# Optimization experiments

Measured on AMD Instinct MI355X. Metric: run time of the kernel, lower is better.

Reference implementation:

```python
import jax, jax.numpy as jnp
import numpy as np

B, S, IN, META, H, G = 256, 1024, 4, 4, 256, 768  # G = 3*H, gate order (r, z, n)


def setup_inputs() -> dict:
    key = jax.random.key(0)
    ks = jax.random.split(key, 12)
    sc = 1.0 / np.sqrt(H)
    return {
        "x": jax.random.normal(ks[0], (B, S, IN), jnp.float32),
        "meta": jax.random.normal(ks[1], (B, META), jnp.float32),
        "W_ih0": jax.random.normal(ks[2], (G, IN + META), jnp.float32) * sc,
        "W_hh0": jax.random.normal(ks[3], (G, H), jnp.float32) * sc,
        "b_ih0": jax.random.normal(ks[4], (G,), jnp.float32) * sc,
        "b_hh0": jax.random.normal(ks[5], (G,), jnp.float32) * sc,
        "W_ih1": jax.random.normal(ks[6], (G, H), jnp.float32) * sc,
        "W_hh1": jax.random.normal(ks[7], (G, H), jnp.float32) * sc,
        "b_ih1": jax.random.normal(ks[8], (G,), jnp.float32) * sc,
        "b_hh1": jax.random.normal(ks[9], (G,), jnp.float32) * sc,
        "fc_W": jax.random.normal(ks[10], (1, H), jnp.float32) * sc,
        "fc_b": jax.random.normal(ks[11], (1,), jnp.float32) * sc,
    }


def _gru_layer(x_seq, W_ih, W_hh, b_ih, b_hh):
    # x_seq: [B, S, F] -> outputs [B, S, H]. PyTorch GRU, gate order (r, z, n).
    h_dim = W_hh.shape[1]
    # Precompute input projections for all timesteps (one big GEMM).
    xg = jnp.einsum('bsf,gf->sbg', x_seq, W_ih) + b_ih  # [S, B, 3H]

    def step(h, xg_t):
        hg = h @ W_hh.T + b_hh  # [B, 3H]
        r = jax.nn.sigmoid(xg_t[:, :h_dim] + hg[:, :h_dim])
        z = jax.nn.sigmoid(xg_t[:, h_dim:2 * h_dim] + hg[:, h_dim:2 * h_dim])
        n = jnp.tanh(xg_t[:, 2 * h_dim:] + r * hg[:, 2 * h_dim:])
        h_new = (1.0 - z) * n + z * h
        return h_new, h_new

    h0 = jnp.zeros((x_seq.shape[0], h_dim), x_seq.dtype)
    _, out = jax.lax.scan(step, h0, xg)  # out: [S, B, H]
    return jnp.transpose(out, (1, 0, 2))


def reference(x, meta, W_ih0, W_hh0, b_ih0, b_hh0, W_ih1, W_hh1, b_ih1, b_hh1, fc_W, fc_b):
    # Tile meta across time and concat to features: [B, S, IN+META]
    meta_t = jnp.broadcast_to(meta[:, None, :], (x.shape[0], x.shape[1], meta.shape[-1]))
    xin = jnp.concatenate([x, meta_t], axis=-1)
    h1 = _gru_layer(xin, W_ih0, W_hh0, b_ih0, b_hh0)
    h2 = _gru_layer(h1, W_ih1, W_hh1, b_ih1, b_hh1)
    last = h2[:, -1, :]  # [B, H]
    return last @ fc_W.T + fc_b  # [B, 1]
```

## Files before the change

### kernel.cpp

```cpp
#include <hip/hip_runtime.h>
#include <hip/hip_fp16.h>


#define SCH 32
#define NCH 32

typedef _Float16 half8 __attribute__((ext_vector_type(8)));
typedef _Float16 half4_t __attribute__((ext_vector_type(4)));
typedef float f32x4 __attribute__((ext_vector_type(4)));

__device__ __forceinline__ float rcp_(float x) {
#if __has_builtin(__builtin_amdgcn_rcpf)
    return __builtin_amdgcn_rcpf(x);
#else
    return 1.f / x;
#endif
}
__device__ __forceinline__ float exp2_(float x) {
#if __has_builtin(__builtin_amdgcn_exp2f)
    return __builtin_amdgcn_exp2f(x);
#else
    return exp2f(x);
#endif
}
__device__ __forceinline__ float sigf(float v) {
    return rcp_(1.f + exp2_(v * -1.442695041f));
}
__device__ __forceinline__ float tanh_(float v) {
    return 1.f - 2.f * rcp_(1.f + exp2_(v * 2.885390082f));
}

__device__ __forceinline__ void lds_barrier() {
    __asm__ volatile("s_waitcnt lgkmcnt(0)" ::: "memory");
    __builtin_amdgcn_s_barrier();
}

__global__ __launch_bounds__(256) void prep_kernel(
    const float* __restrict__ Whh0, const float* __restrict__ Whh1,
    const float* __restrict__ Wih1,
    _Float16* __restrict__ Wfrag0, _Float16* __restrict__ Wfrag1,
    _Float16* __restrict__ Wi1frag) {
    int tid = blockIdx.x * 256 + threadIdx.x;
    int mat = tid / 24576;
    int r   = tid % 24576;
    int kt   = r / 3072;
    int rem  = r % 3072;
    int nt   = rem >> 6;
    int lane = rem & 63;
    int n = nt * 16 + (lane & 15);
    int k = kt * 32 + (lane >> 4) * 8;
    const float* src = (mat == 0 ? Whh0 : (mat == 1 ? Whh1 : Wih1)) + n * 256 + k;
    _Float16* dst = (mat == 0 ? Wfrag0 : (mat == 1 ? Wfrag1 : Wi1frag)) + (size_t)r * 8;
#pragma unroll
    for (int j = 0; j < 8; j++) dst[j] = (_Float16)src[j];
}

__global__
__attribute__((amdgpu_flat_work_group_size(512, 512), amdgpu_waves_per_eu(2, 2)))
void mega_kernel(
    const float* __restrict__ x, const float* __restrict__ meta,
    const float* __restrict__ Wih0, const float* __restrict__ bih0,
    const float* __restrict__ bhh0,
    const _Float16* __restrict__ Wfrag0, const _Float16* __restrict__ Wfrag1,
    const _Float16* __restrict__ Wi1frag,
    const float* __restrict__ bih1, const float* __restrict__ bhh1,
    float* __restrict__ hst0, float* __restrict__ hst1,
    _Float16* __restrict__ hout0, _Float16* __restrict__ hout1,
    _Float16* __restrict__ xg0a, _Float16* __restrict__ xg0b,
    _Float16* __restrict__ xg1a, _Float16* __restrict__ xg1b,
    const float* __restrict__ fcW, const float* __restrict__ fcb,
    float* __restrict__ out, int k) {
    __shared__ __align__(16) char smem[27648];
    const int bid = blockIdx.x;
    const int tid = threadIdx.x;

    if (bid < 64) {
        const int role = bid >> 5;
        const int cc = role ? k - 2 : k;
        if (cc < 0 || cc >= NCH) return;
        const _Float16* Wfrag = role ? Wfrag1 : Wfrag0;
        const float* bhh      = role ? bhh1 : bhh0;
        const _Float16* xgt   = role ? ((cc & 1) ? xg1b : xg1a)
                                     : ((cc & 1) ? xg0b : xg0a);
        float* hstate         = role ? hst1 : hst0;
        _Float16* hof         = (cc & 1) ? hout1 : hout0;
        const bool doHout = (role == 0);
        const bool doFC   = (role == 1) && (cc == NCH - 1);

        _Float16* shA = (_Float16*)smem;
        float* shred  = (float*)smem;
        const int w = tid >> 6, lane = tid & 63;
        const int lm = lane & 15;
        const int hi = lane >> 5;
        const int blk = bid & 31;

        int nt[6];
        nt[0] = 2 * w;      nt[1] = 2 * w + 1;
        nt[2] = 16 + 2 * w; nt[3] = 17 + 2 * w;
        nt[4] = 32 + 2 * w; nt[5] = 33 + 2 * w;

        half8 Bf[48];
#pragma unroll
        for (int kt = 0; kt < 8; kt++)
#pragma unroll
            for (int t = 0; t < 6; t++)
                Bf[kt * 6 + t] = *(const half8*)(Wfrag + (size_t)((kt * 48 + nt[t]) * 64 + lane) * 8);

        const float bbnA = bhh[512 + 32 * w + lm];
        const float bbnB = bhh[512 + 32 * w + 16 + lm];

        float hreg[4];
        if (cc == 0) {
#pragma unroll
            for (int r = 0; r < 4; r++) hreg[r] = 0.f;
        } else {
            f32x4 v0 = *(const f32x4*)(hstate + ((size_t)(blk * 8 + w) * 64 + lane) * 4);
#pragma unroll
            for (int r = 0; r < 4; r++) hreg[r] = v0[r];
        }

        const int rdo = (lane >> 4) * 64 + (lane & 7) * 8;
        const int wb2 = w * 256 + (hi * 2 + (lm >> 3)) * 64 + ((lane >> 4) & 1) * 32 + (lm & 7);

#pragma unroll
        for (int r = 0; r < 4; r++) shA[wb2 + r * 8] = (_Float16)hreg[r];

        const _Float16* xp = xgt + (size_t)(blk * 8 + w) * 768 + lane * 4;
        _Float16* hop = hof + (size_t)(blk * 8 + w) * 256 + lane * 8;

        half4_t xcb[2][3];
        xcb[0][0] = *(const half4_t*)(xp);
        xcb[0][1] = *(const half4_t*)(xp + 256);
        xcb[0][2] = *(const half4_t*)(xp + 512);
        xp += 196608;

        __syncthreads();

#define GRU_STEP(SIDE)                                                            \
    {                                                                             \
        xcb[(SIDE) ^ 1][0] = *(const half4_t*)(xp);                               \
        xcb[(SIDE) ^ 1][1] = *(const half4_t*)(xp + 256);                         \
        xcb[(SIDE) ^ 1][2] = *(const half4_t*)(xp + 512);                         \
        xp += 196608;                                                             \
        f32x4 acc[6];                                                             \
        acc[0] = acc[1] = acc[2] = acc[3] = (f32x4){0.f, 0.f, 0.f, 0.f};          \
        acc[4] = (f32x4){bbnA, bbnA, bbnA, bbnA};                                 \
        acc[5] = (f32x4){bbnB, bbnB, bbnB, bbnB};                                 \
        _Pragma("unroll")                                                         \
        for (int kt = 0; kt < 8; kt++) {                                          \
            half8 af = *(const half8*)(shA + (SIDE) * 2048 + kt * 256 + rdo);     \
            _Pragma("unroll")                                                     \
            for (int t = 0; t < 6; t++)                                           \
                acc[t] = __builtin_amdgcn_mfma_f32_16x16x32_f16(                  \
                    af, Bf[kt * 6 + t], acc[t], 0, 0, 0);                         \
        }                                                                         \
        f32x4 aR = hi ? acc[1] : acc[0];                                          \
        f32x4 aZ = hi ? acc[3] : acc[2];                                          \
        f32x4 aN = hi ? acc[5] : acc[4];                                          \
        half4_t xR = xcb[SIDE][0];                                                \
        half4_t xZ = xcb[SIDE][1];                                                \
        half4_t xN = xcb[SIDE][2];                                                \
        _Pragma("unroll")                                                         \
        for (int r = 0; r < 4; r++) {                                             \
            float rr = sigf((float)xR[r] + aR[r]);                                \
            float zz = sigf((float)xZ[r] + aZ[r]);                                \
            float nn = tanh_((float)xN[r] + rr * aN[r]);                          \
            hreg[r] = nn + zz * (hreg[r] - nn);                                   \
        }                                                                         \
        _Pragma("unroll")                                                         \
        for (int r = 0; r < 4; r++)                                               \
            shA[((SIDE) ^ 1) * 2048 + wb2 + r * 8] = (_Float16)hreg[r];           \
        if (doHout && lane < 32) {                                                \
            half8 v = *(const half8*)(shA + ((SIDE) ^ 1) * 2048 +                 \
                                      w * 256 + lane * 8);                        \
            *(half8*)hop = v;                                                     \
        }                                                                         \
        hop += 65536;                                                             \
        lds_barrier();                                                            \
    }

        for (int s2 = 0; s2 < SCH; s2 += 2) {
            GRU_STEP(0);
            GRU_STEP(1);
        }
#undef GRU_STEP

        {
            f32x4 v0;
#pragma unroll
            for (int r = 0; r < 4; r++) v0[r] = hreg[r];
            *(f32x4*)(hstate + ((size_t)(blk * 8 + w) * 64 + lane) * 4) = v0;
        }

        if (doFC) {
            float fw = fcW[32 * w + hi * 16 + lm];
            f32x4 pv;
#pragma unroll
            for (int r = 0; r < 4; r++) pv[r] = hreg[r] * fw;
            __syncthreads();
            *(f32x4*)(shred + (size_t)(w * 64 + lane) * 4) = pv;
            __syncthreads();
            if (tid < 8) {
                int qq = tid >> 2, rr2 = tid & 3;
                float a = fcb[0];
                for (int ww = 0; ww < 8; ww++)
                    for (int l2 = 0; l2 < 16; l2++)
                        a += shred[(ww * 64 + qq * 16 + l2) * 4 + rr2]
                           + shred[(ww * 64 + 32 + qq * 16 + l2) * 4 + rr2];
                out[blk * 8 + tid] = a;
            }
        }
    } else if (bid < 96) {
        const int cb = k + 1;
        if (cb < 0 || cb >= NCH) return;
        _Float16* xg0 = (cb & 1) ? xg0b : xg0a;
        const int fb = bid - 64;
        float* Wb = (float*)smem;
        for (int i = tid; i < 6912; i += 512)
            Wb[i] = (i < 6144) ? Wih0[i]
                               : (bih0[i - 6144] + ((i - 6144) < 512 ? bhh0[i - 6144] : 0.f));
        __syncthreads();
        const int sub = tid >> 8;
        const int t = tid & 255;
        const int w = t >> 5, l32 = t & 31;
        const int qc = l32 >> 4, lm = l32 & 15;

        float Wr[6][8], br[6];
#pragma unroll
        for (int g3 = 0; g3 < 3; g3++)
#pragma unroll
            for (int tp = 0; tp < 2; tp++) {
                int n = g3 * 256 + 32 * w + 16 * tp + lm;
                int j6 = g3 * 2 + tp;
#pragma unroll
                for (int kk = 0; kk < 8; kk++) Wr[j6][kk] = Wb[n * 8 + kk];
                br[j6] = Wb[6144 + n];
            }
        const int b0 = fb * 8 + qc * 4;
        float4 mv[4];
#pragma unroll
        for (int r = 0; r < 4; r++) mv[r] = *(const float4*)(meta + (b0 + r) * 4);

        for (int sl = 0; sl < 16; sl++) {
            int s_local = sub * 16 + sl;
            int s = cb * SCH + s_local;
            float4 xv[4];
#pragma unroll
            for (int r = 0; r < 4; r++)
                xv[r] = *(const float4*)(x + ((size_t)(b0 + r) * 1024 + s) * 4);
            half4_t o[2][3];
#pragma unroll
            for (int g3 = 0; g3 < 3; g3++)
#pragma unroll
                for (int tp = 0; tp < 2; tp++) {
                    int j6 = g3 * 2 + tp;
#pragma unroll
                    for (int r = 0; r < 4; r++) {
                        float v = br[j6]
                            + xv[r].x * Wr[j6][0] + xv[r].y * Wr[j6][1]
                            + xv[r].z * Wr[j6][2] + xv[r].w * Wr[j6][3]
                            + mv[r].x * Wr[j6][4] + mv[r].y * Wr[j6][5]
                            + mv[r].z * Wr[j6][6] + mv[r].w * Wr[j6][7];
                        o[tp][g3][r] = (_Float16)v;
                    }
                }
            _Float16* dst = xg0 + ((size_t)(s_local * 32 + fb) * 8 + w) * 768;
#pragma unroll
            for (int tp = 0; tp < 2; tp++) {
                int slot4 = (l32 + tp * 32) * 4;
#pragma unroll
                for (int g3 = 0; g3 < 3; g3++)
                    *(half4_t*)(dst + g3 * 256 + slot4) = o[tp][g3];
            }
        }
    } else {
        const int c1 = k - 1;
        if (c1 < 0 || c1 >= NCH) return;
        const _Float16* hof = (c1 & 1) ? hout1 : hout0;
        _Float16* xg1 = (c1 & 1) ? xg1b : xg1a;
        const int fb = bid - 96;
        const int sub = tid >> 8;
        const int t = tid & 255;
        const int wv = t >> 6, lane = t & 63;
        const int q = lane >> 4, lm = lane & 15;
        const int asel = (lane >> 3) & 1;
        const int cidx = (lane >> 4) * 8 + (lane & 7);

        float bias[12];
#pragma unroll
        for (int j = 0; j < 12; j++) {
            int n = (wv * 12 + j) * 16 + lm;
            bias[j] = bih1[n] + (n < 512 ? bhh1[n] : 0.f);
        }
        const int t16 = (fb * 2 + sub) * 2;
        f32x4 acc[2][12] = {};
#pragma unroll
        for (int kt = 0; kt < 8; kt++) {
            half8 af[2], bf[12];
#pragma unroll
            for (int i = 0; i < 2; i++) {
                int tt = t16 + i, s = tt >> 4, bt = tt & 15;
                af[i] = *(const half8*)(hof +
                    (((size_t)(s * 32 + bt * 2 + asel) * 8 + kt) * 32 + cidx) * 8);
            }
#pragma unroll
            for (int j = 0; j < 12; j++)
                bf[j] = *(const half8*)(Wi1frag + (size_t)((kt * 48 + wv * 12 + j) * 64 + lane) * 8);
#pragma unroll
            for (int i = 0; i < 2; i++)
#pragma unroll
                for (int j = 0; j < 12; j++)
                    acc[i][j] = __builtin_amdgcn_mfma_f32_16x16x32_f16(af[i], bf[j], acc[i][j], 0, 0, 0);
        }
#pragma unroll
        for (int i = 0; i < 2; i++) {
            int tt = t16 + i, s = tt >> 4, bt = tt & 15;
            int blk = bt * 2 + (q >> 1), qc2 = q & 1;
#pragma unroll
            for (int j = 0; j < 12; j++) {
                int n = (wv * 12 + j) * 16 + lm;
                int g3 = n >> 8, nn = n & 255;
                int wc = nn >> 5, tp = (nn >> 4) & 1, lmc = nn & 15;
                half4_t v;
#pragma unroll
                for (int r = 0; r < 4; r++) v[r] = (_Float16)(acc[i][j][r] + bias[j]);
                *(half4_t*)(xg1 + ((size_t)(s * 32 + blk) * 8 + wc) * 768
                                 + g3 * 256 + (qc2 * 16 + lmc + tp * 32) * 4) = v;
            }
        }
    }
}

extern "C" void kernel_launch(void* const* d_in, const int* in_sizes, int n_in,
                              void* d_out, int out_size, void* d_ws, size_t ws_size,
                              hipStream_t stream) {
    const float* x    = (const float*)d_in[0];
    const float* meta = (const float*)d_in[1];
    const float* Wih0 = (const float*)d_in[2];
    const float* Whh0 = (const float*)d_in[3];
    const float* bih0 = (const float*)d_in[4];
    const float* bhh0 = (const float*)d_in[5];
    const float* Wih1 = (const float*)d_in[6];
    const float* Whh1 = (const float*)d_in[7];
    const float* bih1 = (const float*)d_in[8];
    const float* bhh1 = (const float*)d_in[9];
    const float* fcW  = (const float*)d_in[10];
    const float* fcb  = (const float*)d_in[11];
    float* out = (float*)d_out;

    char* ws = (char*)d_ws;
    _Float16* Wfrag0  = (_Float16*)(ws + 0);
    _Float16* Wfrag1  = (_Float16*)(ws + 393216);
    _Float16* Wi1frag = (_Float16*)(ws + 786432);
    float*    hst0    = (float*)(ws + 1179648);
    float*    hst1    = (float*)(ws + 1441792);
    _Float16* hout0   = (_Float16*)(ws + 1703936);
    _Float16* xg0a    = (_Float16*)(ws + 5898240);
    _Float16* xg0b    = (_Float16*)(ws + 18481152);
    _Float16* xg1a    = (_Float16*)(ws + 31064064);
    _Float16* xg1b    = (_Float16*)(ws + 43646976);
    _Float16* hout1   = (_Float16*)(ws + 56229888);

    prep_kernel<<<288, 256, 0, stream>>>(Whh0, Whh1, Wih1, Wfrag0, Wfrag1, Wi1frag);

    for (int k = -1; k <= NCH + 1; k++) {
        mega_kernel<<<224, 512, 0, stream>>>(
            x, meta, Wih0, bih0, bhh0, Wfrag0, Wfrag1, Wi1frag, bih1, bhh1,
            hst0, hst1, hout0, hout1, xg0a, xg0b, xg1a, xg1b, fcW, fcb, out, k);
    }
}
```

Before: 1.660 ms.

## Split MFMA accumulator chains and write hidden state directly from registers

The recurrent step now splits the K-loop into two independent accumulator sets, so the dependent MFMA chain is half as long, and sums them afterward. Layer-0 hidden outputs are written by every lane straight from registers in the accumulator layout, instead of being read back from LDS by half the lanes. The layer-1 input-projection blocks stage their hidden tile into padded shared memory to turn the A-operand loads into LDS reads. This trades a few extra vector adds and a larger LDS footprint for a shorter critical path per step and simpler global access.

After: 2.870 ms. 72.9% more time.

```diff
diff --git a/kernel.cpp b/kernel.cpp
--- a/kernel.cpp
+++ b/kernel.cpp
@@ -70,7 +70,7 @@
     _Float16* __restrict__ xg1a, _Float16* __restrict__ xg1b,
     const float* __restrict__ fcW, const float* __restrict__ fcb,
     float* __restrict__ out, int k) {
-    __shared__ __align__(16) char smem[27648];
+    __shared__ __align__(16) char smem[33792];
     const int bid = blockIdx.x;
     const int tid = threadIdx.x;
 
@@ -126,7 +126,7 @@
         for (int r = 0; r < 4; r++) shA[wb2 + r * 8] = (_Float16)hreg[r];
 
         const _Float16* xp = xgt + (size_t)(blk * 8 + w) * 768 + lane * 4;
-        _Float16* hop = hof + (size_t)(blk * 8 + w) * 256 + lane * 8;
+        _Float16* hop = hof + (size_t)(blk * 8 + w) * 256 + lane * 4;
 
         half4_t xcb[2][3];
         xcb[0][0] = *(const half4_t*)(xp);
@@ -142,21 +142,31 @@
         xcb[(SIDE) ^ 1][1] = *(const half4_t*)(xp + 256);                         \
         xcb[(SIDE) ^ 1][2] = *(const half4_t*)(xp + 512);                         \
         xp += 196608;                                                             \
-        f32x4 acc[6];                                                             \
-        acc[0] = acc[1] = acc[2] = acc[3] = (f32x4){0.f, 0.f, 0.f, 0.f};          \
-        acc[4] = (f32x4){bbnA, bbnA, bbnA, bbnA};                                 \
-        acc[5] = (f32x4){bbnB, bbnB, bbnB, bbnB};                                 \
+        f32x4 aA[6], aB[6];                                                       \
+        aA[0] = aA[1] = aA[2] = aA[3] = (f32x4){0.f, 0.f, 0.f, 0.f};              \
+        aA[4] = (f32x4){bbnA, bbnA, bbnA, bbnA};                                  \
+        aA[5] = (f32x4){bbnB, bbnB, bbnB, bbnB};                                  \
+        aB[0] = aB[1] = aB[2] = aB[3] = (f32x4){0.f, 0.f, 0.f, 0.f};              \
+        aB[4] = aB[5] = (f32x4){0.f, 0.f, 0.f, 0.f};                              \
         _Pragma("unroll")                                                         \
-        for (int kt = 0; kt < 8; kt++) {                                          \
+        for (int kt = 0; kt < 4; kt++) {                                          \
             half8 af = *(const half8*)(shA + (SIDE) * 2048 + kt * 256 + rdo);     \
             _Pragma("unroll")                                                     \
             for (int t = 0; t < 6; t++)                                           \
-                acc[t] = __builtin_amdgcn_mfma_f32_16x16x32_f16(                  \
-                    af, Bf[kt * 6 + t], acc[t], 0, 0, 0);                         \
+                aA[t] = __builtin_amdgcn_mfma_f32_16x16x32_f16(                   \
+                    af, Bf[kt * 6 + t], aA[t], 0, 0, 0);                          \
         }                                                                         \
-        f32x4 aR = hi ? acc[1] : acc[0];                                          \
-        f32x4 aZ = hi ? acc[3] : acc[2];                                          \
-        f32x4 aN = hi ? acc[5] : acc[4];                                          \
+        _Pragma("unroll")                                                         \
+        for (int kt = 4; kt < 8; kt++) {                                          \
+            half8 af = *(const half8*)(shA + (SIDE) * 2048 + kt * 256 + rdo);     \
+            _Pragma("unroll")                                                     \
+            for (int t = 0; t < 6; t++)                                           \
+                aB[t] = __builtin_amdgcn_mfma_f32_16x16x32_f16(                   \
+                    af, Bf[kt * 6 + t], aB[t], 0, 0, 0);                          \
+        }                                                                         \
+        f32x4 aR = (hi ? aA[1] : aA[0]) + (hi ? aB[1] : aB[0]);                   \
+        f32x4 aZ = (hi ? aA[3] : aA[2]) + (hi ? aB[3] : aB[2]);                   \
+        f32x4 aN = (hi ? aA[5] : aA[4]) + (hi ? aB[5] : aB[4]);                   \
         half4_t xR = xcb[SIDE][0];                                                \
         half4_t xZ = xcb[SIDE][1];                                                \
         half4_t xN = xcb[SIDE][2];                                                \
@@ -170,10 +180,11 @@
         _Pragma("unroll")                                                         \
         for (int r = 0; r < 4; r++)                                               \
             shA[((SIDE) ^ 1) * 2048 + wb2 + r * 8] = (_Float16)hreg[r];           \
-        if (doHout && lane < 32) {                                                \
-            half8 v = *(const half8*)(shA + ((SIDE) ^ 1) * 2048 +                 \
-                                      w * 256 + lane * 8);                        \
-            *(half8*)hop = v;                                                     \
+        if (doHout) {                                                             \
+            half4_t hv;                                                           \
+            _Pragma("unroll")                                                     \
+            for (int r = 0; r < 4; r++) hv[r] = (_Float16)hreg[r];                \
+            *(half4_t*)hop = hv;                                                  \
         }                                                                         \
         hop += 65536;                                                             \
         lds_barrier();                                                            \
@@ -279,12 +290,28 @@
         const _Float16* hof = (c1 & 1) ? hout1 : hout0;
         _Float16* xg1 = (c1 & 1) ? xg1b : xg1a;
         const int fb = bid - 96;
-        const int sub = tid >> 8;
+        const int s_ch = fb >> 2;
+        const int bb8 = (fb & 3) * 8;
+        _Float16* Ah = (_Float16*)smem;
+
+#pragma unroll
+        for (int i = 0; i < 8; i++) {
+            int u = i * 512 + tid;
+            int rq = u >> 8, c = u & 255;
+            int blk8 = bb8 + (rq >> 1), qh = rq & 1;
+            int wc = c >> 5, hic = (c >> 4) & 1, lmc = c & 15;
+            half4_t hv = *(const half4_t*)(hof +
+                (((size_t)(s_ch * 32 + blk8) * 8 + wc) * 64 + hic * 32 + qh * 16 + lmc) * 4);
+#pragma unroll
+            for (int r2 = 0; r2 < 4; r2++)
+                Ah[(rq * 4 + r2) * 264 + c] = hv[r2];
+        }
+        __syncthreads();
+
+        const int th = tid >> 8;
         const int t = tid & 255;
         const int wv = t >> 6, lane = t & 63;
         const int q = lane >> 4, lm = lane & 15;
-        const int asel = (lane >> 3) & 1;
-        const int cidx = (lane >> 4) * 8 + (lane & 7);
 
         float bias[12];
 #pragma unroll
@@ -292,17 +319,13 @@
             int n = (wv * 12 + j) * 16 + lm;
             bias[j] = bih1[n] + (n < 512 ? bhh1[n] : 0.f);
         }
-        const int t16 = (fb * 2 + sub) * 2;
         f32x4 acc[2][12] = {};
 #pragma unroll
         for (int kt = 0; kt < 8; kt++) {
             half8 af[2], bf[12];
 #pragma unroll
-            for (int i = 0; i < 2; i++) {
-                int tt = t16 + i, s = tt >> 4, bt = tt & 15;
-                af[i] = *(const half8*)(hof +
-                    (((size_t)(s * 32 + bt * 2 + asel) * 8 + kt) * 32 + cidx) * 8);
-            }
+            for (int i = 0; i < 2; i++)
+                af[i] = *(const half8*)(&Ah[((th * 2 + i) * 16 + lm) * 264 + kt * 32 + q * 8]);
 #pragma unroll
             for (int j = 0; j < 12; j++)
                 bf[j] = *(const half8*)(Wi1frag + (size_t)((kt * 48 + wv * 12 + j) * 64 + lane) * 8);
@@ -314,18 +337,18 @@
         }
 #pragma unroll
         for (int i = 0; i < 2; i++) {
-            int tt = t16 + i, s = tt >> 4, bt = tt & 15;
-            int blk = bt * 2 + (q >> 1), qc2 = q & 1;
+            int tt = fb * 4 + th * 2 + i, s = tt >> 4, bt = tt & 15;
+            int blkw = bt * 2 + (q >> 1), qc2 = q & 1;
 #pragma unroll
             for (int j = 0; j < 12; j++) {
                 int n = (wv * 12 + j) * 16 + lm;
                 int g3 = n >> 8, nn = n & 255;
-                int wc = nn >> 5, tp = (nn >> 4) & 1, lmc = nn & 15;
+                int wc2 = nn >> 5, tp = (nn >> 4) & 1, lmc2 = nn & 15;
                 half4_t v;
 #pragma unroll
                 for (int r = 0; r < 4; r++) v[r] = (_Float16)(acc[i][j][r] + bias[j]);
-                *(half4_t*)(xg1 + ((size_t)(s * 32 + blk) * 8 + wc) * 768
-                                 + g3 * 256 + (qc2 * 16 + lmc + tp * 32) * 4) = v;
+                *(half4_t*)(xg1 + ((size_t)(s * 32 + blkw) * 8 + wc2) * 768
+                                 + g3 * 256 + (qc2 * 16 + lmc2 + tp * 32) * 4) = v;
             }
         }
     }
```
